# Kernel tuning notes

Measured on AMD Instinct MI355X. Metric: run time of the kernel, lower is better.

The kernel has to match this reference:

```python
import jax, jax.numpy as jnp
import numpy as np

B, L, D = 1, 4096, 1024
H, HD = 16, 64

def setup_inputs() -> dict:
    key = jax.random.key(0)
    ks = jax.random.split(key, 5)
    scale = 1.0 / np.sqrt(D)
    return {
        "x": jax.random.normal(ks[0], (B, L, D), dtype=jnp.float32),
        "Wq": jax.random.normal(ks[1], (D, D), dtype=jnp.float32) * scale,
        "Wk": jax.random.normal(ks[2], (D, D), dtype=jnp.float32) * scale,
        "Wv": jax.random.normal(ks[3], (D, D), dtype=jnp.float32) * scale,
        "Wo": jax.random.normal(ks[4], (D, D), dtype=jnp.float32) * scale,
    }

def reference(x, Wq, Wk, Wv, Wo):
    Bc, Lc, _ = x.shape
    # torch Linear: y = x @ W.T
    q = (x @ Wq.T).reshape(Bc, Lc, H, HD).transpose(0, 2, 1, 3)  # [B,H,L,hd]
    k = (x @ Wk.T).reshape(Bc, Lc, H, HD).transpose(0, 2, 1, 3)
    v = (x @ Wv.T).reshape(Bc, Lc, H, HD).transpose(0, 2, 1, 3)
    scale = HD ** -0.5
    scores = jnp.einsum('bhqd,bhkd->bhqk', q, k) * scale  # [B,H,L,L]
    causal = jnp.tril(jnp.ones((Lc, Lc), dtype=bool))
    scores = jnp.where(causal, scores, -jnp.inf)
    attn = jax.nn.softmax(scores, axis=-1)
    out = jnp.einsum('bhqk,bhkd->bhqd', attn, v)
    out = out.transpose(0, 2, 1, 3).reshape(Bc, Lc, H * HD)
    return out @ Wo.T
```

## Files before the change

### kernel.cpp

```cpp
#include <hip/hip_runtime.h>
#include <hip/hip_bf16.h>
#include <stdint.h>

#define L_SEQ   4096
#define D_MODEL 1024
#define N_HEADS 16
#define HEAD_DIM 64

typedef uint16_t u16;
typedef __bf16 bf16x8 __attribute__((ext_vector_type(8)));
typedef short s16x4 __attribute__((ext_vector_type(4)));
typedef float floatx4 __attribute__((ext_vector_type(4)));

__device__ __forceinline__ floatx4 mfma32(bf16x8 a, bf16x8 b, floatx4 c) {
  return __builtin_amdgcn_mfma_f32_16x16x32_bf16(a, b, c, 0, 0, 0);
}

__device__ __forceinline__ floatx4 mfma16(s16x4 a, s16x4 b, floatx4 c) {
#if __has_builtin(__builtin_amdgcn_mfma_f32_16x16x16bf16_1k)
  return __builtin_amdgcn_mfma_f32_16x16x16bf16_1k(a, b, c, 0, 0, 0);
#else
  floatx4 d;
  asm volatile("v_mfma_f32_16x16x16_bf16 %0, %1, %2, %3"
               : "=v"(d) : "v"(a), "v"(b), "v"(c));
  return d;
#endif
}

__device__ __forceinline__ float hw_exp2(float x) {
  return __builtin_amdgcn_exp2f(x);
}

__device__ __forceinline__ uint32_t fbits(float f) {
  union { float f; uint32_t u; } x; x.f = f; return x.u;
}

__device__ __forceinline__ uint32_t pack_bf16_trunc(float f1, float f0) {
  return __builtin_amdgcn_perm(fbits(f1), fbits(f0), 0x07060302u);
}

__device__ __forceinline__ void load16_lds(const u16* g, u16* l) {
  __builtin_amdgcn_global_load_lds(
      (const __attribute__((address_space(1))) void*)g,
      (__attribute__((address_space(3))) void*)l, 16, 0, 0);
}

__device__ __forceinline__ u16 f2bf(float f) {
  uint32_t u = fbits(f);
  uint32_t r = u + 0x7FFFu + ((u >> 16) & 1u);
  return (u16)(r >> 16);
}

#define Q_PRESCALE 0.18033688011112042f

__global__ __launch_bounds__(256) void cvt_kernel(
    const float* __restrict__ x,  const float* __restrict__ wq,
    const float* __restrict__ wk, const float* __restrict__ wv,
    const float* __restrict__ wo,
    u16* __restrict__ xb, u16* __restrict__ wqb, u16* __restrict__ wkb,
    u16* __restrict__ wvb, u16* __restrict__ wob) {
  const int z = blockIdx.z;
  const float* s; u16* d; int n;
  if (z == 0)      { s = x;  d = xb;  n = L_SEQ * D_MODEL; }
  else if (z == 1) { s = wq; d = wqb; n = D_MODEL * D_MODEL; }
  else if (z == 2) { s = wk; d = wkb; n = D_MODEL * D_MODEL; }
  else if (z == 3) { s = wv; d = wvb; n = D_MODEL * D_MODEL; }
  else             { s = wo; d = wob; n = D_MODEL * D_MODEL; }
  const int stride = gridDim.x * 256 * 4;
  for (int i = (blockIdx.x * 256 + threadIdx.x) * 4; i < n; i += stride) {
    float4 v = *(const float4*)(s + i);
    ushort4 o;
    o.x = f2bf(v.x); o.y = f2bf(v.y); o.z = f2bf(v.z); o.w = f2bf(v.w);
    *(ushort4*)(d + i) = o;
  }
}

__global__ __launch_bounds__(256) void qkv_gemm_kernel(
    const u16* __restrict__ X,
    const u16* __restrict__ Wq, const u16* __restrict__ Wk, const u16* __restrict__ Wv,
    u16* __restrict__ Qo, u16* __restrict__ Ko, u16* __restrict__ VTo) {
  constexpr int BK = 32, Kdim = D_MODEL;
  __shared__ __align__(16) u16 As[128 * BK];
  __shared__ __align__(16) u16 Bs[128 * BK];

  const int z = blockIdx.z;
  const u16* __restrict__ A;
  const u16* __restrict__ B;
  int m0, n0;
  if (z < 2) { A = X; B = z ? Wk : Wq; m0 = blockIdx.x * 128; n0 = blockIdx.y * 128; }
  else       { A = Wv; B = X;          m0 = blockIdx.y * 128; n0 = blockIdx.x * 128; }

  const int tid = threadIdx.x;
  const int wave = tid >> 6, lane = tid & 63;
  const int wm = wave & 1, wn = wave >> 1;
  const int quad = lane >> 4, l15 = lane & 15;

  floatx4 acc[4][4] = {};

  const int cbase = wave * 128;
  const int c0 = cbase + lane, c1 = c0 + 64;
  const int r0 = c0 >> 2, cc0 = (c0 & 3) * 8;
  const int r1 = c1 >> 2, cc1 = (c1 & 3) * 8;

  for (int k0 = 0; k0 < Kdim; k0 += BK) {
    load16_lds(&A[(size_t)(m0 + r0) * Kdim + k0 + cc0], &As[cbase * 8]);
    load16_lds(&A[(size_t)(m0 + r1) * Kdim + k0 + cc1], &As[(cbase + 64) * 8]);
    load16_lds(&B[(size_t)(n0 + r0) * Kdim + k0 + cc0], &Bs[cbase * 8]);
    load16_lds(&B[(size_t)(n0 + r1) * Kdim + k0 + cc1], &Bs[(cbase + 64) * 8]);
    __syncthreads();

    bf16x8 af[4], wf[4];
#pragma unroll
    for (int i = 0; i < 4; ++i)
      af[i] = *(const bf16x8*)(&As[(wm * 64 + i * 16 + l15) * BK + quad * 8]);
#pragma unroll
    for (int j = 0; j < 4; ++j)
      wf[j] = *(const bf16x8*)(&Bs[(wn * 64 + j * 16 + l15) * BK + quad * 8]);
#pragma unroll
    for (int i = 0; i < 4; ++i)
#pragma unroll
      for (int j = 0; j < 4; ++j)
        acc[i][j] = mfma32(af[i], wf[j], acc[i][j]);
    __syncthreads();
  }

  const float scale = (z == 0) ? Q_PRESCALE : 1.0f;
  u16* __restrict__ C = (z == 0) ? Qo : (z == 1) ? Ko : VTo;
#pragma unroll
  for (int i = 0; i < 4; ++i) {
    const int mb = m0 + wm * 64 + i * 16 + quad * 4;
#pragma unroll
    for (int j = 0; j < 4; ++j) {
      const int n = n0 + wn * 64 + j * 16 + l15;
#pragma unroll
      for (int r = 0; r < 4; ++r) {
        const int m = mb + r;
        if (z < 2) {
          C[(size_t)(n >> 6) * (size_t)L_SEQ * HEAD_DIM + (size_t)m * HEAD_DIM + (n & 63)] =
              f2bf(acc[i][j][r] * scale);
        } else {
          C[(size_t)(m >> 6) * (size_t)L_SEQ * HEAD_DIM + (size_t)(m & 63) * L_SEQ + n] =
              f2bf(acc[i][j][r]);
        }
      }
    }
  }
}

__global__ __launch_bounds__(256) void out_gemm_kernel(
    const u16* __restrict__ A, const u16* __restrict__ W, float* __restrict__ C) {
  constexpr int BK = 32, Kdim = D_MODEL;
  __shared__ __align__(16) u16 As[128 * BK];
  __shared__ __align__(16) u16 Bs[64 * BK];

  const int tid = threadIdx.x;
  const int wave = tid >> 6, lane = tid & 63;
  const int wm = wave & 1, wn = wave >> 1;
  const int quad = lane >> 4, l15 = lane & 15;
  const int m0 = blockIdx.x * 128, n0 = blockIdx.y * 64;

  floatx4 acc[4][2] = {};

  const int cbase = wave * 128;
  const int c0 = cbase + lane, c1 = c0 + 64;
  const int ra0 = c0 >> 2, ca0 = (c0 & 3) * 8;
  const int ra1 = c1 >> 2, ca1 = (c1 & 3) * 8;
  const int cb = wave * 64 + lane;
  const int rb = cb >> 2, cbcol = (cb & 3) * 8;

  for (int k0 = 0; k0 < Kdim; k0 += BK) {
    load16_lds(&A[(size_t)(m0 + ra0) * Kdim + k0 + ca0], &As[cbase * 8]);
    load16_lds(&A[(size_t)(m0 + ra1) * Kdim + k0 + ca1], &As[(cbase + 64) * 8]);
    load16_lds(&W[(size_t)(n0 + rb) * Kdim + k0 + cbcol], &Bs[wave * 64 * 8]);
    __syncthreads();

    bf16x8 af[4], wf[2];
#pragma unroll
    for (int i = 0; i < 4; ++i)
      af[i] = *(const bf16x8*)(&As[(wm * 64 + i * 16 + l15) * BK + quad * 8]);
#pragma unroll
    for (int j = 0; j < 2; ++j)
      wf[j] = *(const bf16x8*)(&Bs[(wn * 32 + j * 16 + l15) * BK + quad * 8]);
#pragma unroll
    for (int i = 0; i < 4; ++i)
#pragma unroll
      for (int j = 0; j < 2; ++j)
        acc[i][j] = mfma32(af[i], wf[j], acc[i][j]);
    __syncthreads();
  }

#pragma unroll
  for (int i = 0; i < 4; ++i) {
    const int mb = m0 + wm * 64 + i * 16 + quad * 4;
#pragma unroll
    for (int j = 0; j < 2; ++j) {
      const int n = n0 + wn * 32 + j * 16 + l15;
#pragma unroll
      for (int r = 0; r < 4; ++r)
        C[(size_t)(mb + r) * D_MODEL + n] = acc[i][j][r];
    }
  }
}

#define LDP 72
__global__ __launch_bounds__(256, 3) void attn_kernel(
    const u16* __restrict__ Q, const u16* __restrict__ K,
    const u16* __restrict__ VT, u16* __restrict__ Oa) {
  __shared__ __align__(16) u16 Vts[64 * LDP];
  __shared__ __align__(16) float Of[4 * 64 * 16];
  __shared__ float Lf[4 * 64 + 64];

  const int b = blockIdx.x;
  const int h = (b & 7) * 2 + (b >> 8);
  const int pair = (b >> 3) & 31;
  const int tid = threadIdx.x;
  const int wave = tid >> 6, lane = tid & 63;
  const int quad = lane >> 4, l15 = lane & 15;

  const size_t hoff = (size_t)h * L_SEQ * HEAD_DIM;
  const u16* __restrict__ Qh = Q + hoff;
  const u16* __restrict__ Kh = K + hoff;
  const u16* __restrict__ VTh = VT + hoff;

  const u16* const Kg = Kh + (size_t)(wave * 16 + l15) * HEAD_DIM;
  const int vd0 = lane >> 1, vk = (lane & 1) * 8;
  u16* const VsW0 = &Vts[vd0 * LDP + wave * 16 + vk];
  u16* const VsW1 = &Vts[(vd0 + 32) * LDP + wave * 16 + vk];
  const u16* const Vg0 = VTh + (size_t)vd0 * L_SEQ + wave * 16 + vk;
  const u16* const Vg1 = VTh + (size_t)(vd0 + 32) * L_SEQ + wave * 16 + vk;

  for (int half = 0; half < 2; ++half) {
    const int qt = half ? (63 - pair) : pair;
    const int q0 = qt * 64;

    bf16x8 qf[4][2];
#pragma unroll
    for (int jq = 0; jq < 4; ++jq) {
      const u16* qrow = Qh + (size_t)(q0 + jq * 16 + l15) * HEAD_DIM;
      qf[jq][0] = *(const bf16x8*)(qrow + quad * 8);
      qf[jq][1] = *(const bf16x8*)(qrow + 32 + quad * 8);
    }

    floatx4 oacc[4][4] = {};
    float psum[4] = {};

    bf16x8 kc0 = *(const bf16x8*)(Kg + quad * 8);
    bf16x8 kc1 = *(const bf16x8*)(Kg + 32 + quad * 8);
    float4 va  = *(const float4*)(Vg0);
    float4 vb4 = *(const float4*)(Vg1);

    for (int kt = 0; kt <= qt; ++kt) {
      *(float4*)VsW0 = va;
      *(float4*)VsW1 = vb4;
      bf16x8 kf0 = kc0, kf1 = kc1;
      if (kt < qt) {
        const u16* Kn = Kg + (size_t)(kt + 1) * 64 * HEAD_DIM;
        kc0 = *(const bf16x8*)(Kn + quad * 8);
        kc1 = *(const bf16x8*)(Kn + 32 + quad * 8);
        va  = *(const float4*)(Vg0 + (size_t)(kt + 1) * 64);
        vb4 = *(const float4*)(Vg1 + (size_t)(kt + 1) * 64);
      }

      floatx4 s[4];
#pragma unroll
      for (int jq = 0; jq < 4; ++jq) {
        floatx4 z = {};
        z = mfma32(kf0, qf[jq][0], z);
        z = mfma32(kf1, qf[jq][1], z);
        s[jq] = z;
      }

      if (kt == qt) {
        const int keyw = wave * 16 + quad * 4;
#pragma unroll
        for (int jq = 0; jq < 4; ++jq) {
          const int qloc = jq * 16 + l15;
#pragma unroll
          for (int r = 0; r < 4; ++r)
            if (keyw + r > qloc) s[jq][r] = -1e30f;
        }
      }

      s16x4 pa[4];
#pragma unroll
      for (int jq = 0; jq < 4; ++jq) {
        float p0 = hw_exp2(s[jq][0]);
        float p1 = hw_exp2(s[jq][1]);
        float p2 = hw_exp2(s[jq][2]);
        float p3 = hw_exp2(s[jq][3]);
        psum[jq] += (p0 + p1) + (p2 + p3);
        union { uint32_t w[2]; s16x4 v; } pu;
        pu.w[0] = pack_bf16_trunc(p1, p0);
        pu.w[1] = pack_bf16_trunc(p3, p2);
        pa[jq] = pu.v;
      }

      s16x4 vb[4];
#pragma unroll
      for (int nt = 0; nt < 4; ++nt)
        vb[nt] = *(const s16x4*)(&Vts[(nt * 16 + l15) * LDP + wave * 16 + quad * 4]);
#pragma unroll
      for (int jq = 0; jq < 4; ++jq)
#pragma unroll
        for (int nt = 0; nt < 4; ++nt)
          oacc[jq][nt] = mfma16(pa[jq], vb[nt], oacc[jq][nt]);
    }

#pragma unroll
    for (int jq = 0; jq < 4; ++jq) {
      psum[jq] += __shfl_xor(psum[jq], 16, 64);
      psum[jq] += __shfl_xor(psum[jq], 32, 64);
    }
    if (quad == 0) {
#pragma unroll
      for (int jq = 0; jq < 4; ++jq)
        Lf[wave * 64 + jq * 16 + l15] = psum[jq];
    }
    __syncthreads();
    if (tid < 64) {
      float lt = Lf[tid] + Lf[64 + tid] + Lf[128 + tid] + Lf[192 + tid];
      Lf[256 + tid] = 1.0f / lt;
    }

    const int qc = tid >> 2, d4 = (tid & 3) * 4;
#pragma unroll
    for (int nt = 0; nt < 4; ++nt) {
#pragma unroll
      for (int jq = 0; jq < 4; ++jq)
#pragma unroll
        for (int r = 0; r < 4; ++r)
          Of[wave * 1024 + (jq * 16 + quad * 4 + r) * 16 + l15] = oacc[jq][nt][r];
      __syncthreads();
      const float invq = Lf[256 + qc];
      floatx4 a0 = *(const floatx4*)&Of[0 * 1024 + qc * 16 + d4];
      floatx4 a1 = *(const floatx4*)&Of[1 * 1024 + qc * 16 + d4];
      floatx4 a2 = *(const floatx4*)&Of[2 * 1024 + qc * 16 + d4];
      floatx4 a3 = *(const floatx4*)&Of[3 * 1024 + qc * 16 + d4];
      floatx4 sum = (a0 + a1) + (a2 + a3);
      ushort4 o;
      o.x = f2bf(sum[0] * invq); o.y = f2bf(sum[1] * invq);
      o.z = f2bf(sum[2] * invq); o.w = f2bf(sum[3] * invq);
      *(ushort4*)(Oa + (size_t)(q0 + qc) * D_MODEL + (size_t)h * HEAD_DIM +
                  nt * 16 + d4) = o;
      __syncthreads();
    }
  }
}

extern "C" void kernel_launch(void* const* d_in, const int* in_sizes, int n_in,
                              void* d_out, int out_size, void* d_ws, size_t ws_size,
                              hipStream_t stream) {
  const float* x  = (const float*)d_in[0];
  const float* Wq = (const float*)d_in[1];
  const float* Wk = (const float*)d_in[2];
  const float* Wv = (const float*)d_in[3];
  const float* Wo = (const float*)d_in[4];
  float* out = (float*)d_out;

  const size_t XN = (size_t)L_SEQ * D_MODEL;
  const size_t WN = (size_t)D_MODEL * D_MODEL;
  const size_t HLHD = (size_t)N_HEADS * L_SEQ * HEAD_DIM;

  u16* x_bf  = (u16*)d_ws;
  u16* wq_bf = x_bf + XN;
  u16* wk_bf = wq_bf + WN;
  u16* wv_bf = wk_bf + WN;
  u16* wo_bf = wv_bf + WN;
  u16* q_ws  = wo_bf + WN;
  u16* k_ws  = q_ws + HLHD;
  u16* vT_ws = k_ws + HLHD;
  u16* a_ws  = vT_ws + HLHD;

  dim3 gc(1024, 1, 5);
  cvt_kernel<<<gc, 256, 0, stream>>>(x, Wq, Wk, Wv, Wo,
                                     x_bf, wq_bf, wk_bf, wv_bf, wo_bf);

  dim3 gqkv(L_SEQ / 128, D_MODEL / 128, 3);
  qkv_gemm_kernel<<<gqkv, 256, 0, stream>>>(x_bf, wq_bf, wk_bf, wv_bf,
                                            q_ws, k_ws, vT_ws);

  dim3 ga(512, 1, 1);
  attn_kernel<<<ga, 256, 0, stream>>>(q_ws, k_ws, vT_ws, a_ws);

  dim3 go(L_SEQ / 128, D_MODEL / 64, 1);
  out_gemm_kernel<<<go, 256, 0, stream>>>(a_ws, wo_bf, out);
}
```

Before: 202.1 us.

## Double-buffer LDS in projection GEMMs and swizzle QKV block order

Both projection GEMMs now use two LDS buffers. The next K-tile is issued before the current tile's MFMAs run, which drops one barrier per iteration and overlaps global-to-LDS loads with compute. The QKV GEMM also moves to a 1D grid whose block index is remapped so that the 8 consecutive blocks (b&7) cover different output tiles, presumably spreading work across the XCDs and improving L2 reuse. This doubles LDS use per block, which may lower occupancy.

New measurement: 196.5 us. -2.8%, faster.

```diff
diff --git a/kernel.cpp b/kernel.cpp
--- a/kernel.cpp
+++ b/kernel.cpp
@@ -79,16 +79,21 @@
     const u16* __restrict__ X,
     const u16* __restrict__ Wq, const u16* __restrict__ Wk, const u16* __restrict__ Wv,
     u16* __restrict__ Qo, u16* __restrict__ Ko, u16* __restrict__ VTo) {
-  constexpr int BK = 32, Kdim = D_MODEL;
-  __shared__ __align__(16) u16 As[128 * BK];
-  __shared__ __align__(16) u16 Bs[128 * BK];
-
-  const int z = blockIdx.z;
+  constexpr int BK = 32, Kdim = D_MODEL, NIT = Kdim / BK;
+  __shared__ __align__(16) u16 As[2][128 * BK];
+  __shared__ __align__(16) u16 Bs[2][128 * BK];
+
+  const int b = blockIdx.x;
+  const int g = b & 7, i2 = b >> 3;
+  const int z = i2 % 3, j = i2 / 3;
+  const int x = (g & 3) * 8 + (j & 7);
+  const int y = (g >> 2) * 4 + (j >> 3);
+
   const u16* __restrict__ A;
   const u16* __restrict__ B;
   int m0, n0;
-  if (z < 2) { A = X; B = z ? Wk : Wq; m0 = blockIdx.x * 128; n0 = blockIdx.y * 128; }
-  else       { A = Wv; B = X;          m0 = blockIdx.y * 128; n0 = blockIdx.x * 128; }
+  if (z < 2) { A = X; B = z ? Wk : Wq; m0 = x * 128; n0 = y * 128; }
+  else       { A = Wv; B = X;          m0 = y * 128; n0 = x * 128; }
 
   const int tid = threadIdx.x;
   const int wave = tid >> 6, lane = tid & 63;
@@ -102,26 +107,32 @@
   const int r0 = c0 >> 2, cc0 = (c0 & 3) * 8;
   const int r1 = c1 >> 2, cc1 = (c1 & 3) * 8;
 
-  for (int k0 = 0; k0 < Kdim; k0 += BK) {
-    load16_lds(&A[(size_t)(m0 + r0) * Kdim + k0 + cc0], &As[cbase * 8]);
-    load16_lds(&A[(size_t)(m0 + r1) * Kdim + k0 + cc1], &As[(cbase + 64) * 8]);
-    load16_lds(&B[(size_t)(n0 + r0) * Kdim + k0 + cc0], &Bs[cbase * 8]);
-    load16_lds(&B[(size_t)(n0 + r1) * Kdim + k0 + cc1], &Bs[(cbase + 64) * 8]);
+  auto stage = [&](int k0, int sel) {
+    load16_lds(&A[(size_t)(m0 + r0) * Kdim + k0 + cc0], &As[sel][cbase * 8]);
+    load16_lds(&A[(size_t)(m0 + r1) * Kdim + k0 + cc1], &As[sel][(cbase + 64) * 8]);
+    load16_lds(&B[(size_t)(n0 + r0) * Kdim + k0 + cc0], &Bs[sel][cbase * 8]);
+    load16_lds(&B[(size_t)(n0 + r1) * Kdim + k0 + cc1], &Bs[sel][(cbase + 64) * 8]);
+  };
+
+  stage(0, 0);
+  for (int kk = 0; kk < NIT; ++kk) {
     __syncthreads();
+    if (kk + 1 < NIT) stage((kk + 1) * BK, (kk + 1) & 1);
+    const u16* Asc = As[kk & 1];
+    const u16* Bsc = Bs[kk & 1];
 
     bf16x8 af[4], wf[4];
 #pragma unroll
     for (int i = 0; i < 4; ++i)
-      af[i] = *(const bf16x8*)(&As[(wm * 64 + i * 16 + l15) * BK + quad * 8]);
-#pragma unroll
-    for (int j = 0; j < 4; ++j)
-      wf[j] = *(const bf16x8*)(&Bs[(wn * 64 + j * 16 + l15) * BK + quad * 8]);
+      af[i] = *(const bf16x8*)(&Asc[(wm * 64 + i * 16 + l15) * BK + quad * 8]);
+#pragma unroll
+    for (int jn = 0; jn < 4; ++jn)
+      wf[jn] = *(const bf16x8*)(&Bsc[(wn * 64 + jn * 16 + l15) * BK + quad * 8]);
 #pragma unroll
     for (int i = 0; i < 4; ++i)
 #pragma unroll
-      for (int j = 0; j < 4; ++j)
-        acc[i][j] = mfma32(af[i], wf[j], acc[i][j]);
-    __syncthreads();
+      for (int jn = 0; jn < 4; ++jn)
+        acc[i][jn] = mfma32(af[i], wf[jn], acc[i][jn]);
   }
 
   const float scale = (z == 0) ? Q_PRESCALE : 1.0f;
@@ -130,17 +141,17 @@
   for (int i = 0; i < 4; ++i) {
     const int mb = m0 + wm * 64 + i * 16 + quad * 4;
 #pragma unroll
-    for (int j = 0; j < 4; ++j) {
-      const int n = n0 + wn * 64 + j * 16 + l15;
+    for (int jn = 0; jn < 4; ++jn) {
+      const int n = n0 + wn * 64 + jn * 16 + l15;
 #pragma unroll
       for (int r = 0; r < 4; ++r) {
         const int m = mb + r;
         if (z < 2) {
           C[(size_t)(n >> 6) * (size_t)L_SEQ * HEAD_DIM + (size_t)m * HEAD_DIM + (n & 63)] =
-              f2bf(acc[i][j][r] * scale);
+              f2bf(acc[i][jn][r] * scale);
         } else {
           C[(size_t)(m >> 6) * (size_t)L_SEQ * HEAD_DIM + (size_t)(m & 63) * L_SEQ + n] =
-              f2bf(acc[i][j][r]);
+              f2bf(acc[i][jn][r]);
         }
       }
     }
@@ -149,9 +160,9 @@
 
 __global__ __launch_bounds__(256) void out_gemm_kernel(
     const u16* __restrict__ A, const u16* __restrict__ W, float* __restrict__ C) {
-  constexpr int BK = 32, Kdim = D_MODEL;
-  __shared__ __align__(16) u16 As[128 * BK];
-  __shared__ __align__(16) u16 Bs[64 * BK];
+  constexpr int BK = 32, Kdim = D_MODEL, NIT = Kdim / BK;
+  __shared__ __align__(16) u16 As[2][128 * BK];
+  __shared__ __align__(16) u16 Bs[2][64 * BK];
 
   const int tid = threadIdx.x;
   const int wave = tid >> 6, lane = tid & 63;
@@ -168,36 +179,42 @@
   const int cb = wave * 64 + lane;
   const int rb = cb >> 2, cbcol = (cb & 3) * 8;
 
-  for (int k0 = 0; k0 < Kdim; k0 += BK) {
-    load16_lds(&A[(size_t)(m0 + ra0) * Kdim + k0 + ca0], &As[cbase * 8]);
-    load16_lds(&A[(size_t)(m0 + ra1) * Kdim + k0 + ca1], &As[(cbase + 64) * 8]);
-    load16_lds(&W[(size_t)(n0 + rb) * Kdim + k0 + cbcol], &Bs[wave * 64 * 8]);
+  auto stage = [&](int k0, int sel) {
+    load16_lds(&A[(size_t)(m0 + ra0) * Kdim + k0 + ca0], &As[sel][cbase * 8]);
+    load16_lds(&A[(size_t)(m0 + ra1) * Kdim + k0 + ca1], &As[sel][(cbase + 64) * 8]);
+    load16_lds(&W[(size_t)(n0 + rb) * Kdim + k0 + cbcol], &Bs[sel][wave * 64 * 8]);
+  };
+
+  stage(0, 0);
+  for (int kk = 0; kk < NIT; ++kk) {
     __syncthreads();
+    if (kk + 1 < NIT) stage((kk + 1) * BK, (kk + 1) & 1);
+    const u16* Asc = As[kk & 1];
+    const u16* Bsc = Bs[kk & 1];
 
     bf16x8 af[4], wf[2];
 #pragma unroll
     for (int i = 0; i < 4; ++i)
-      af[i] = *(const bf16x8*)(&As[(wm * 64 + i * 16 + l15) * BK + quad * 8]);
-#pragma unroll
-    for (int j = 0; j < 2; ++j)
-      wf[j] = *(const bf16x8*)(&Bs[(wn * 32 + j * 16 + l15) * BK + quad * 8]);
+      af[i] = *(const bf16x8*)(&Asc[(wm * 64 + i * 16 + l15) * BK + quad * 8]);
+#pragma unroll
+    for (int jn = 0; jn < 2; ++jn)
+      wf[jn] = *(const bf16x8*)(&Bsc[(wn * 32 + jn * 16 + l15) * BK + quad * 8]);
 #pragma unroll
     for (int i = 0; i < 4; ++i)
 #pragma unroll
-      for (int j = 0; j < 2; ++j)
-        acc[i][j] = mfma32(af[i], wf[j], acc[i][j]);
-    __syncthreads();
+      for (int jn = 0; jn < 2; ++jn)
+        acc[i][jn] = mfma32(af[i], wf[jn], acc[i][jn]);
   }
 
 #pragma unroll
   for (int i = 0; i < 4; ++i) {
     const int mb = m0 + wm * 64 + i * 16 + quad * 4;
 #pragma unroll
-    for (int j = 0; j < 2; ++j) {
-      const int n = n0 + wn * 32 + j * 16 + l15;
+    for (int jn = 0; jn < 2; ++jn) {
+      const int n = n0 + wn * 32 + jn * 16 + l15;
 #pragma unroll
       for (int r = 0; r < 4; ++r)
-        C[(size_t)(mb + r) * D_MODEL + n] = acc[i][j][r];
+        C[(size_t)(mb + r) * D_MODEL + n] = acc[i][jn][r];
     }
   }
 }
@@ -375,7 +392,7 @@
   cvt_kernel<<<gc, 256, 0, stream>>>(x, Wq, Wk, Wv, Wo,
                                      x_bf, wq_bf, wk_bf, wv_bf, wo_bf);
 
-  dim3 gqkv(L_SEQ / 128, D_MODEL / 128, 3);
+  dim3 gqkv(768, 1, 1);
   qkv_gemm_kernel<<<gqkv, 256, 0, stream>>>(x_bf, wq_bf, wk_bf, wv_bf,
                                             q_ws, k_ws, vT_ws);
 
```
